# Optimization experiments

Hardware: AMD Instinct MI355X
Metric: run time of the kernel (lower is better)

The kernel has to match this reference:

```python
import jax, jax.numpy as jnp
import numpy as np

B, N, D, K = 4, 4096, 64, 16
SCALE = float(np.sqrt(D))


def setup_inputs() -> dict:
    key = jax.random.key(0)
    ks = jax.random.split(key, 16)
    f = lambda i, shape: jax.random.normal(ks[i], shape, dtype=jnp.float32) * 0.05
    return {
        'x': jax.random.normal(ks[0], (B, N, D), dtype=jnp.float32),
        'pos': jax.random.uniform(ks[1], (B, N, 3), dtype=jnp.float32),
        'Wq': f(2, (D, D)), 'Wk': f(3, (D, D)), 'Wv': f(4, (D, D)),
        'P1': f(5, (3, D)), 'p1b': f(6, (D,)), 'P2': f(7, (D, D)), 'p2b': f(8, (D,)),
        'A1': f(9, (D, D)), 'a1b': f(10, (D,)), 'A2': f(11, (D, D)), 'a2b': f(12, (D,)),
        'Wf': f(13, (D, D)), 'bf': f(14, (D,)),
    }


def _gather(feats, idx):
    # feats: [B,N,C], idx: [B,N,K] -> [B,N,K,C]  (index_points / idx_pt)
    return jax.vmap(lambda f, i: f[i])(feats, idx)


def reference(x, pos, Wq, Wk, Wv, P1, p1b, P2, p2b, A1, a1b, A2, a2b, Wf, bf):
    # kNN via squared distances (same math as square_distance + argsort[:, :, :k])
    sq = jnp.sum(pos * pos, axis=-1)                                   # [B,N]
    dists = sq[:, :, None] + sq[:, None, :] - 2.0 * jnp.einsum('bnc,bmc->bnm', pos, pos)
    _, idx = jax.lax.top_k(-dists, K)                                  # [B,N,K]

    knn_xyz = _gather(pos, idx)                                        # [B,N,K,3]
    q = x @ Wq                                                         # [B,N,D]
    kf = _gather(x @ Wk, idx)                                          # [B,N,K,D]
    v = _gather(x @ Wv, idx)                                           # [B,N,K,D]

    rel = pos[:, :, None, :] - knn_xyz                                 # [B,N,K,3]
    pos_enc = jax.nn.relu(rel @ P1 + p1b) @ P2 + p2b                   # [B,N,K,D]

    attn = jax.nn.relu((q[:, :, None, :] - kf + pos_enc) @ A1 + a1b) @ A2 + a2b
    attn = jax.nn.softmax(attn / SCALE, axis=-2)                       # softmax over K

    agg = jnp.sum(attn * (v + pos_enc), axis=2)                        # [B,N,D]
    return agg @ Wf + bf + x                                           # residual
```

## Files before the change

### kernel.cpp

```cpp
#include <hip/hip_runtime.h>
#include <hip/hip_bf16.h>
#include <stdint.h>

#define B_ 4
#define N_ 4096
#define D_ 64
#define K_ 16

static const size_t OFS_WQA1  = 0;
static const size_t OFS_WKA1  = 4096;
static const size_t OFS_WCOMB = 8192;
static const size_t OFS_C1    = 16384;
static const size_t OFS_QA1   = 16448;
static const size_t OFS_KA1   = OFS_QA1 + (size_t)B_*N_*64;
static const size_t OFS_V     = OFS_KA1 + (size_t)B_*N_*64;
static const size_t OFS_IDX   = OFS_V   + (size_t)B_*N_*64;
static const size_t OFS_POS4  = OFS_IDX + (size_t)B_*N_*16;
static const size_t OFS_BF16  = OFS_POS4 + (size_t)B_*N_*4;
static const size_t OFS_PBF   = OFS_BF16 + 6144;
static const size_t OFS_WFB   = OFS_PBF + 6144;
static const size_t OFS_APK   = OFS_WFB + 2048;
static const size_t OFS_BPK   = OFS_APK + 262144;

#define KNN_CAP 96

typedef __attribute__((ext_vector_type(8))) short short8;
typedef __attribute__((ext_vector_type(4))) float floatx4;

__device__ __forceinline__ unsigned short f2bf(float f) {
    __hip_bfloat16 h = __float2bfloat16(f);
    return *reinterpret_cast<unsigned short*>(&h);
}

__device__ __forceinline__ float bf2f(unsigned short u) {
    __hip_bfloat16 h = *reinterpret_cast<__hip_bfloat16*>(&u);
    return __bfloat162float(h);
}

__device__ __forceinline__ unsigned long long bsortu64(unsigned long long v, int l) {
#pragma unroll
    for (int k = 2; k <= 64; k <<= 1) {
#pragma unroll
        for (int j = k >> 1; j > 0; j >>= 1) {
            unsigned long long o = __shfl_xor(v, j, 64);
            unsigned long long mn = v < o ? v : o;
            unsigned long long mx = v < o ? o : v;
            v = ((((l & j) == 0) == ((l & k) == 0))) ? mn : mx;
        }
    }
    return v;
}

__device__ __forceinline__ void bsortu64x2(unsigned long long& a, unsigned long long& b, int l) {
#pragma unroll
    for (int k = 2; k <= 64; k <<= 1) {
#pragma unroll
        for (int j = k >> 1; j > 0; j >>= 1) {
            unsigned long long oa = __shfl_xor(a, j, 64);
            unsigned long long ob = __shfl_xor(b, j, 64);
            bool up = (((l & j) == 0) == ((l & k) == 0));
            unsigned long long mna = a < oa ? a : oa, mxa = a < oa ? oa : a;
            unsigned long long mnb = b < ob ? b : ob, mxb = b < ob ? ob : b;
            a = up ? mna : mxa;
            b = up ? mnb : mxb;
        }
    }
}

__global__ __launch_bounds__(256) void k_pre(
        const float* __restrict__ Wq, const float* __restrict__ Wk,
        const float* __restrict__ Wv, const float* __restrict__ Wf,
        const float* __restrict__ P2, const float* __restrict__ A1,
        const float* __restrict__ p2b, const float* __restrict__ a1b,
        const float* __restrict__ pos, float* __restrict__ ws) {
    int blk = blockIdx.x;
    unsigned short* pbf = (unsigned short*)(ws + OFS_PBF);
    if (blk < 65) {
        int i = blk * 256 + threadIdx.x;
        if (i < 4096) {
            int c = i >> 6, d = i & 63;
            float s = 0.f;
            for (int e = 0; e < 64; ++e) s = fmaf(Wq[c*64+e], A1[e*64+d], s);
            ws[OFS_WQA1 + i] = s;
            pbf[d*64 + c] = f2bf(s);
        } else if (i < 8192) {
            int j = i - 4096; int c = j >> 6, d = j & 63;
            float s = 0.f;
            for (int e = 0; e < 64; ++e) s = fmaf(Wk[c*64+e], A1[e*64+d], s);
            ws[OFS_WKA1 + j] = s;
            pbf[(64+d)*64 + c] = f2bf(s);
        } else if (i < 16384) {
            int j = i - 8192; int c = j >> 7, dd = j & 127;
            float s;
            if (dd < 64) { s = 0.f; for (int e = 0; e < 64; ++e) s = fmaf(P2[c*64+e], A1[e*64+dd], s); }
            else s = P2[c*64 + (dd - 64)];
            ws[OFS_WCOMB + j] = s;
        } else if (i < 16448) {
            int d = i - 16384;
            float s = a1b[d];
            for (int e = 0; e < 64; ++e) s = fmaf(p2b[e], A1[e*64+d], s);
            ws[OFS_C1 + d] = s;
        }
    } else if (blk < 81) {
        int i = (blk - 65) * 256 + threadIdx.x;
        int c = i >> 6, d = i & 63;
        pbf[(128+d)*64 + c] = f2bf(Wv[c*64+d]);
    } else if (blk < 97) {
        int i = (blk - 81) * 256 + threadIdx.x;
        int c = i >> 6, d = i & 63;
        ((unsigned short*)(ws + OFS_WFB))[d*64 + c] = f2bf(Wf[c*64+d]);
    } else {
        int i = (blk - 97) * 256 + threadIdx.x;
        float px = pos[(size_t)i*3+0], py = pos[(size_t)i*3+1], pz = pos[(size_t)i*3+2];
        float sq = fmaf(pz, pz, fmaf(py, py, px*px));
        ((float4*)(ws + OFS_POS4))[i] = make_float4(px, py, pz, sq);

        unsigned short xh = f2bf(px), yh = f2bf(py), zh = f2bf(pz), sh = f2bf(sq);
        float xl = px - bf2f(xh), yl = py - bf2f(yh), zl = pz - bf2f(zh), sl = sq - bf2f(sh);
        unsigned short xlb = f2bf(xl), ylb = f2bf(yl), zlb = f2bf(zl), slb = f2bf(sl);
        unsigned short m2xh = f2bf(-2.f*bf2f(xh)), m2yh = f2bf(-2.f*bf2f(yh)), m2zh = f2bf(-2.f*bf2f(zh));
        unsigned short m2xl = f2bf(-2.f*xl), m2yl = f2bf(-2.f*yl), m2zl = f2bf(-2.f*zl);
        const unsigned short ONE = 0x3F80;
        union { unsigned short u[32]; uint4 v[4]; } A, Bp;
#pragma unroll
        for (int j2 = 0; j2 < 32; ++j2) { A.u[j2] = 0; Bp.u[j2] = 0; }
        A.u[0]=m2xh; A.u[1]=m2xh; A.u[2]=m2xl;
        A.u[3]=m2yh; A.u[4]=m2yh; A.u[5]=m2yl;
        A.u[6]=m2zh; A.u[7]=m2zh; A.u[8]=m2zl;
        A.u[9]=sh;   A.u[10]=slb; A.u[11]=ONE; A.u[12]=ONE;
        Bp.u[0]=xh;  Bp.u[1]=xlb; Bp.u[2]=xh;
        Bp.u[3]=yh;  Bp.u[4]=ylb; Bp.u[5]=yh;
        Bp.u[6]=zh;  Bp.u[7]=zlb; Bp.u[8]=zh;
        Bp.u[9]=ONE; Bp.u[10]=ONE; Bp.u[11]=sh; Bp.u[12]=slb;
        uint4* ap4 = (uint4*)(ws + OFS_APK);
        uint4* bp4 = (uint4*)(ws + OFS_BPK);
#pragma unroll
        for (int j2 = 0; j2 < 4; ++j2) { ap4[(size_t)i*4+j2] = A.v[j2]; bp4[(size_t)i*4+j2] = Bp.v[j2]; }
    }
}

__global__ __launch_bounds__(256) void k_projm(const float* __restrict__ x,
                                               const float* __restrict__ A2,
                                               float* __restrict__ ws) {
    __shared__ unsigned short xT[64*72];
    __shared__ unsigned short wTs[192*72];
    const int t = threadIdx.x;
    if (blockIdx.x >= 256) {
        int i = ((int)blockIdx.x - 256) * 256 + t;
        unsigned short* wbf = (unsigned short*)(ws + OFS_BF16);
        if (i < 8192) {
            int c = i >> 7, dd = i & 127;
            wbf[dd*64 + c] = f2bf(ws[OFS_WCOMB + i]);
        } else {
            int j = i - 8192; int e = j >> 6, d = j & 63;
            wbf[8192 + d*64 + e] = f2bf(A2[j]);
        }
        return;
    }
    const unsigned short* pbf = (const unsigned short*)(ws + OFS_PBF);
    const int g0 = (int)blockIdx.x * 64;

#pragma unroll
    for (int k = 0; k < 6; ++k) {
        int id  = t + 256*k;
        int row = id >> 3, cir = id & 7;
        uint4 vv = *(const uint4*)(pbf + row*64 + cir*8);
        *(uint4*)&wTs[row*72 + cir*8] = vv;
    }
    {
        int r = t >> 2, qd = t & 3;
        const float* src = x + (size_t)(g0 + r)*64 + qd*16;
        unsigned short hb[16];
#pragma unroll
        for (int u = 0; u < 16; ++u) hb[u] = f2bf(src[u]);
        *(uint4*)&xT[r*72 + qd*16]     = *(uint4*)&hb[0];
        *(uint4*)&xT[r*72 + qd*16 + 8] = *(uint4*)&hb[8];
    }
    __syncthreads();

    const int w = t >> 6, l = t & 63, lr = l & 15, q = l >> 4;
    floatx4 acc[12];
#pragma unroll
    for (int j = 0; j < 12; ++j) acc[j] = (floatx4){0.f, 0.f, 0.f, 0.f};
#pragma unroll
    for (int kb = 0; kb < 2; ++kb) {
        short8 a = *(const short8*)&xT[(16*w + lr)*72 + 32*kb + 8*q];
#pragma unroll
        for (int j = 0; j < 12; ++j) {
            short8 bfr = *(const short8*)&wTs[(16*j + lr)*72 + 32*kb + 8*q];
            acc[j] = __builtin_amdgcn_mfma_f32_16x16x32_bf16(a, bfr, acc[j], 0, 0, 0);
        }
    }
    float* qA1 = ws + OFS_QA1;
    float* kA1 = ws + OFS_KA1;
    float* vws = ws + OFS_V;
#pragma unroll
    for (int j = 0; j < 12; ++j) {
        int col = 16*j + lr;
        float* dst = (col < 64) ? qA1 : (col < 128 ? kA1 : vws);
        int c2 = col & 63;
#pragma unroll
        for (int r = 0; r < 4; ++r) {
            int grow = g0 + 16*w + 4*q + r;
            dst[(size_t)grow*64 + c2] = acc[j][r];
        }
    }
}

__device__ __forceinline__ unsigned long long knn_pack_entry4(
        const float4 q4, const float4* __restrict__ pos4b,
        const unsigned* __restrict__ lists,
        int a1, int a2, int a3, int T, int e) {
    bool valid = e < T;
    int s = (e >= a1) + (e >= a2) + (e >= a3);
    int base = (s == 0) ? 0 : ((s == 1) ? a1 : ((s == 2) ? a2 : a3));
    int off = e - base;
    off = off < 0 ? 0 : (off > KNN_CAP-1 ? KNN_CAP-1 : off);
    unsigned idxv = lists[s*KNN_CAP + off];
    idxv = valid ? (idxv & 4095u) : 0u;
    float4 c4 = pos4b[idxv];
    float dot = fmaf(q4.z, c4.z, fmaf(q4.y, c4.y, q4.x*c4.x));
    float d = fmaxf(fmaf(-2.f, dot, q4.w + c4.w), 0.f);
    unsigned long long pk = ((unsigned long long)__float_as_uint(d) << 32) | idxv;
    return valid ? pk : ~0ull;
}

__device__ __forceinline__ unsigned long long knn_merge_rest4(
        unsigned long long best, int l, const float4 q4,
        const float4* __restrict__ pos4b, const unsigned* __restrict__ lists,
        int a1, int a2, int a3, int T) {
    for (int base = 64; base < T; base += 64) {
        unsigned long long w2 = knn_pack_entry4(q4, pos4b, lists, a1, a2, a3, T, base + l);
        w2 = bsortu64(w2, l);
        unsigned long long bb = __shfl(w2, (l - 16) & 63, 64);
        unsigned long long nv = (l < 16) ? best : ((l < 32) ? bb : ~0ull);
        best = bsortu64(nv, l);
    }
    return best;
}

__global__ __launch_bounds__(256) void k_knn(float* __restrict__ ws) {
    __shared__ unsigned surv[16*4*KNN_CAP];
    __shared__ int scnt[64];
    const unsigned short* apk = (const unsigned short*)(ws + OFS_APK);
    const unsigned short* bpk = (const unsigned short*)(ws + OFS_BPK);
    const int t = threadIdx.x;
    const int w = t >> 6, l = t & 63;
    const int lr = l & 15, hi4 = l >> 4;
    const int g0 = (int)blockIdx.x * 16;
    const int b  = g0 >> 12;

    short8 afrag = *(const short8*)(apk + (size_t)(g0 + lr)*32 + 8*hi4);
    const unsigned short* bbase = bpk + (size_t)(b*4096 + w*1024 + lr)*32 + 8*hi4;
    const floatx4 z4 = {0.f, 0.f, 0.f, 0.f};

    float run1[4], run2[4];
#pragma unroll
    for (int r = 0; r < 4; ++r) { run1[r] = 1e30f; run2[r] = 1e30f; }
    {
        short8 cur[4], nxt[4];
#pragma unroll
        for (int u = 0; u < 4; ++u) cur[u] = *(const short8*)(bbase + u*512);
#pragma unroll 4
        for (int g = 0; g < 16; ++g) {
            const int gn = ((g + 1) & 15) * 4;
#pragma unroll
            for (int u = 0; u < 4; ++u) nxt[u] = *(const short8*)(bbase + (gn+u)*512);
#pragma unroll
            for (int u = 0; u < 4; ++u) {
                floatx4 a = __builtin_amdgcn_mfma_f32_16x16x32_bf16(afrag, cur[u], z4, 0, 0, 0);
#pragma unroll
                for (int r = 0; r < 4; ++r) {
                    run2[r] = fminf(run2[r], fmaxf(run1[r], a[r]));
                    run1[r] = fminf(run1[r], a[r]);
                }
            }
#pragma unroll
            for (int u = 0; u < 4; ++u) cur[u] = nxt[u];
        }
    }

    float tau[4];
#pragma unroll
    for (int r = 0; r < 4; ++r) {
        float v = run2[r];
#pragma unroll
        for (int k = 2; k <= 16; k <<= 1) {
#pragma unroll
            for (int j = k >> 1; j > 0; j >>= 1) {
                float o = __shfl_xor(v, j, 64);
                bool up = (((lr & j) == 0) == ((lr & k) == 0));
                v = up ? fminf(v, o) : fmaxf(v, o);
            }
        }
        tau[r] = __shfl(v, (l & 48) | 7, 64) + 1e-3f;
    }

    int cnt[4] = {0, 0, 0, 0};
    const unsigned lm16 = (1u << lr) - 1u;
    unsigned su[4];
#pragma unroll
    for (int r = 0; r < 4; ++r) su[r] = (unsigned)(((4*hi4 + r)*4 + w) * KNN_CAP);
    const unsigned cand0 = (unsigned)(w*1024 + lr);
    {
        short8 cur[4], nxt[4];
#pragma unroll
        for (int u = 0; u < 4; ++u) cur[u] = *(const short8*)(bbase + u*512);
#pragma unroll 4
        for (int g = 0; g < 16; ++g) {
            const int gn = ((g + 1) & 15) * 4;
#pragma unroll
            for (int u = 0; u < 4; ++u) nxt[u] = *(const short8*)(bbase + (gn+u)*512);
#pragma unroll
            for (int u = 0; u < 4; ++u) {
                floatx4 a = __builtin_amdgcn_mfma_f32_16x16x32_bf16(afrag, cur[u], z4, 0, 0, 0);
                unsigned cid = cand0 + (unsigned)((g*4 + u)*16);
#pragma unroll
                for (int r = 0; r < 4; ++r) {
                    bool pred = a[r] <= tau[r];
                    unsigned long long m = __ballot(pred);
                    if (m) {
                        unsigned gm = (unsigned)(m >> (hi4 * 16)) & 0xFFFFu;
                        int pos = cnt[r] + __popc(gm & lm16);
                        if (pred && pos < KNN_CAP) surv[su[r] + pos] = cid;
                        cnt[r] += __popc(gm);
                    }
                }
            }
#pragma unroll
            for (int u = 0; u < 4; ++u) cur[u] = nxt[u];
        }
    }
    if (lr == 0) {
#pragma unroll
        for (int r = 0; r < 4; ++r) scnt[(4*hi4 + r)*4 + w] = cnt[r];
    }
    __syncthreads();

    const float4* pos4g = (const float4*)(ws + OFS_POS4);
    const float4* pos4b = pos4g + (size_t)b * N_;
    int* idx = (int*)(ws + OFS_IDX);
    for (int p = 0; p < 2; ++p) {
        int qa = w*4 + 2*p, qb = qa + 1;
        int ca[4], cb[4];
#pragma unroll
        for (int s = 0; s < 4; ++s) {
            int v0 = scnt[qa*4 + s]; ca[s] = v0 < KNN_CAP ? v0 : KNN_CAP;
            int v1 = scnt[qb*4 + s]; cb[s] = v1 < KNN_CAP ? v1 : KNN_CAP;
        }
        int a1 = ca[0], a2 = a1 + ca[1], a3 = a2 + ca[2], Ta = a3 + ca[3];
        int b1 = cb[0], b2 = b1 + cb[1], b3 = b2 + cb[2], Tb = b3 + cb[3];
        const unsigned* sa = surv + qa*4*KNN_CAP;
        const unsigned* sb = surv + qb*4*KNN_CAP;
        float4 q4a = pos4g[g0 + qa];
        float4 q4b = pos4g[g0 + qb];
        unsigned long long pk0 = knn_pack_entry4(q4a, pos4b, sa, a1, a2, a3, Ta, l);
        unsigned long long pk1 = knn_pack_entry4(q4b, pos4b, sb, b1, b2, b3, Tb, l);
        bsortu64x2(pk0, pk1, l);
        if (Ta > 64) pk0 = knn_merge_rest4(pk0, l, q4a, pos4b, sa, a1, a2, a3, Ta);
        if (Tb > 64) pk1 = knn_merge_rest4(pk1, l, q4b, pos4b, sb, b1, b2, b3, Tb);
        if (l < 16) {
            idx[(size_t)(g0 + qa)*16 + l] = (int)(pk0 & 0xFFFu);
            idx[(size_t)(g0 + qb)*16 + l] = (int)(pk1 & 0xFFFu);
        }
    }
}

__global__ __launch_bounds__(256) void k_attn(
    const float* __restrict__ x, const float* __restrict__ pos,
    const float* __restrict__ P1, const float* __restrict__ p1b,
    const float* __restrict__ p2b, const float* __restrict__ a2b,
    const float* __restrict__ bff, const float* __restrict__ ws,
    float* __restrict__ out) {

    __shared__ unsigned short wT[128*72];
    __shared__ unsigned short a2T[64*72];
    __shared__ unsigned short abuf[128*72];
    __shared__ float relb[128*4];
    __shared__ int   mrow[128];

    const int t  = threadIdx.x;
    const int g0 = blockIdx.x * 8;
    const int b  = g0 >> 12;
    const float* qA1 = ws + OFS_QA1;
    const float* kA1 = ws + OFS_KA1;
    const float* vws = ws + OFS_V;
    const float* c1  = ws + OFS_C1;
    const int* idx = (const int*)(ws + OFS_IDX);
    const unsigned short* wbf = (const unsigned short*)(ws + OFS_BF16);
    const unsigned short* wfb = (const unsigned short*)(ws + OFS_WFB);

#pragma unroll
    for (int k = 0; k < 6; ++k) {
        int id  = t + 256*k;
        int row = id >> 3, cir = id & 7;
        uint4 vv = *(const uint4*)(wbf + row*64 + cir*8);
        if (row < 128) *(uint4*)&wT[row*72 + cir*8] = vv;
        else           *(uint4*)&a2T[(row-128)*72 + cir*8] = vv;
    }

    if (t < 128) {
        int p = t >> 4, k = t & 15;
        int ng = g0 + p;
        int m  = idx[(size_t)ng*16 + k];
        int mg = b * N_ + m;
        mrow[t] = mg;
        relb[t*4+0] = pos[(size_t)ng*3+0] - pos[(size_t)mg*3+0];
        relb[t*4+1] = pos[(size_t)ng*3+1] - pos[(size_t)mg*3+1];
        relb[t*4+2] = pos[(size_t)ng*3+2] - pos[(size_t)mg*3+2];
    }
    __syncthreads();

    const int w = t >> 6, l = t & 63, lr = l & 15, q = l >> 4;

    float kpre[2][4][4];
    float qpre[2][4];
#pragma unroll
    for (int i = 0; i < 2; ++i) {
        int ng = g0 + 2*w + i;
#pragma unroll
        for (int j = 0; j < 4; ++j) {
            int col = 16*j + lr;
            qpre[i][j] = qA1[(size_t)ng*64 + col] + c1[col];
#pragma unroll
            for (int r = 0; r < 4; ++r) {
                int row = 32*w + 16*i + 4*q + r;
                kpre[i][j][r] = kA1[(size_t)mrow[row]*64 + col];
            }
        }
    }

    {
        int d = t & 63, r0 = t >> 6;
        float w0 = P1[d], w1 = P1[64+d], w2 = P1[128+d], bb = p1b[d];
#pragma unroll
        for (int jj = 0; jj < 32; ++jj) {
            int r = r0 + jj*4;
            float h = fmaf(relb[r*4+2], w2, fmaf(relb[r*4+1], w1, fmaf(relb[r*4+0], w0, bb)));
            abuf[r*72 + d] = f2bf(fmaxf(h, 0.f));
        }
    }
    __syncthreads();

    floatx4 acc1[2][8];
#pragma unroll
    for (int i = 0; i < 2; ++i)
#pragma unroll
        for (int j = 0; j < 8; ++j) acc1[i][j] = (floatx4){0.f, 0.f, 0.f, 0.f};
#pragma unroll
    for (int kb = 0; kb < 2; ++kb) {
        short8 a0 = *(const short8*)&abuf[(32*w      + lr)*72 + 32*kb + 8*q];
        short8 a1 = *(const short8*)&abuf[(32*w + 16 + lr)*72 + 32*kb + 8*q];
#pragma unroll
        for (int j = 0; j < 8; ++j) {
            short8 bfr = *(const short8*)&wT[(16*j + lr)*72 + 32*kb + 8*q];
            acc1[0][j] = __builtin_amdgcn_mfma_f32_16x16x32_bf16(a0, bfr, acc1[0][j], 0, 0, 0);
            acc1[1][j] = __builtin_amdgcn_mfma_f32_16x16x32_bf16(a1, bfr, acc1[1][j], 0, 0, 0);
        }
    }
    __syncthreads();

#pragma unroll
    for (int i = 0; i < 2; ++i) {
#pragma unroll
        for (int j = 0; j < 4; ++j) {
            int col = 16*j + lr;
            float qv = qpre[i][j];
#pragma unroll
            for (int r = 0; r < 4; ++r) {
                int row = 32*w + 16*i + 4*q + r;
                float t1 = acc1[i][j][r] + qv - kpre[i][j][r];
                abuf[row*72 + col] = f2bf(fmaxf(t1, 0.f));
            }
        }
    }

    float vpre[2][4][4];
#pragma unroll
    for (int i = 0; i < 2; ++i)
#pragma unroll
        for (int j = 0; j < 4; ++j) {
            int col = 16*j + lr;
#pragma unroll
            for (int r = 0; r < 4; ++r) {
                int row = 32*w + 16*i + 4*q + r;
                vpre[i][j][r] = vws[(size_t)mrow[row]*64 + col];
            }
        }
    short8 wffrag[2];
#pragma unroll
    for (int kb = 0; kb < 2; ++kb)
        wffrag[kb] = *(const short8*)&wfb[(16*w + lr)*64 + 32*kb + 8*q];
    __syncthreads();

    floatx4 acc2[2][4];
#pragma unroll
    for (int i = 0; i < 2; ++i)
#pragma unroll
        for (int j = 0; j < 4; ++j) acc2[i][j] = (floatx4){0.f, 0.f, 0.f, 0.f};
#pragma unroll
    for (int kb = 0; kb < 2; ++kb) {
        short8 a0 = *(const short8*)&abuf[(32*w      + lr)*72 + 32*kb + 8*q];
        short8 a1 = *(const short8*)&abuf[(32*w + 16 + lr)*72 + 32*kb + 8*q];
#pragma unroll
        for (int j = 0; j < 4; ++j) {
            short8 bfr = *(const short8*)&a2T[(16*j + lr)*72 + 32*kb + 8*q];
            acc2[0][j] = __builtin_amdgcn_mfma_f32_16x16x32_bf16(a0, bfr, acc2[0][j], 0, 0, 0);
            acc2[1][j] = __builtin_amdgcn_mfma_f32_16x16x32_bf16(a1, bfr, acc2[1][j], 0, 0, 0);
        }
    }
    __syncthreads();

#pragma unroll
    for (int i = 0; i < 2; ++i) {
#pragma unroll
        for (int j = 0; j < 4; ++j) {
            int col = 16*j + lr;
            float a2bv = a2b[col], p2bv = p2b[col];
            float L[4];
#pragma unroll
            for (int r = 0; r < 4; ++r) L[r] = acc2[i][j][r] + a2bv;
            float mx = fmaxf(fmaxf(L[0], L[1]), fmaxf(L[2], L[3]));
            mx = fmaxf(mx, __shfl_xor(mx, 16, 64));
            mx = fmaxf(mx, __shfl_xor(mx, 32, 64));
            float ssum = 0.f, part = 0.f;
#pragma unroll
            for (int r = 0; r < 4; ++r) {
                float e = __expf((L[r] - mx) * 0.125f);
                ssum += e;
                float wv = vpre[i][j][r] + (acc1[i][4+j][r] + p2bv);
                part = fmaf(e, wv, part);
            }
            ssum += __shfl_xor(ssum, 16, 64);
            ssum += __shfl_xor(ssum, 32, 64);
            part += __shfl_xor(part, 16, 64);
            part += __shfl_xor(part, 32, 64);
            float agg = part / ssum;
            if (q == 0) abuf[(2*w + i)*72 + col] = f2bf(agg);
        }
    }
    __syncthreads();

    {
        floatx4 accF = (floatx4){0.f, 0.f, 0.f, 0.f};
#pragma unroll
        for (int kb = 0; kb < 2; ++kb) {
            short8 afr = *(const short8*)&abuf[lr*72 + 32*kb + 8*q];
            accF = __builtin_amdgcn_mfma_f32_16x16x32_bf16(afr, wffrag[kb], accF, 0, 0, 0);
        }
        if (q < 2) {
            int col = 16*w + lr;
            float bv = bff[col];
#pragma unroll
            for (int r = 0; r < 4; ++r) {
                int g = g0 + 4*q + r;
                out[(size_t)g*64 + col] = accF[r] + bv + x[(size_t)g*64 + col];
            }
        }
    }
}

extern "C" void kernel_launch(void* const* d_in, const int* in_sizes, int n_in,
                              void* d_out, int out_size, void* d_ws, size_t ws_size,
                              hipStream_t stream) {
    const float* x   = (const float*)d_in[0];
    const float* pos = (const float*)d_in[1];
    const float* Wq  = (const float*)d_in[2];
    const float* Wk  = (const float*)d_in[3];
    const float* Wv  = (const float*)d_in[4];
    const float* P1  = (const float*)d_in[5];
    const float* p1b = (const float*)d_in[6];
    const float* P2  = (const float*)d_in[7];
    const float* p2b = (const float*)d_in[8];
    const float* A1  = (const float*)d_in[9];
    const float* a1b = (const float*)d_in[10];
    const float* A2  = (const float*)d_in[11];
    const float* a2b = (const float*)d_in[12];
    const float* Wf  = (const float*)d_in[13];
    const float* bf  = (const float*)d_in[14];
    float* out = (float*)d_out;
    float* ws  = (float*)d_ws;

    hipLaunchKernelGGL(k_pre,   dim3(161),  dim3(256), 0, stream,
                       Wq, Wk, Wv, Wf, P2, A1, p2b, a1b, pos, ws);
    hipLaunchKernelGGL(k_projm, dim3(304),  dim3(256), 0, stream, x, A2, ws);
    hipLaunchKernelGGL(k_knn,   dim3(1024), dim3(256), 0, stream, ws);
    hipLaunchKernelGGL(k_attn,  dim3(2048), dim3(256), 0, stream,
                       x, pos, P1, p1b, p2b, a2b, bf, ws, out);
}
```

Before: 195.2 us.

## Split kNN candidate scan across 8 waves with shared-memory min merge and atomic survivors

The kNN kernel now runs 512 threads, so each of 8 waves scans 512 candidates instead of 4 waves scanning 1024. Per-wave top-2 minima are merged through shared memory to form the threshold. Survivors go into one list per query via LDS atomics instead of per-wave ballot-compacted lists, which removes the 4-list indexing in the final sort. The aim is shorter per-wave serial scans and more parallelism, at the cost of an extra barrier, LDS atomic contention, and the survivor cap now applying to the whole list rather than to each wave's list.

```diff
diff --git a/kernel.cpp b/kernel.cpp
--- a/kernel.cpp
+++ b/kernel.cpp
@@ -207,16 +207,12 @@
     }
 }
 
-__device__ __forceinline__ unsigned long long knn_pack_entry4(
+__device__ __forceinline__ unsigned long long knn_entry(
         const float4 q4, const float4* __restrict__ pos4b,
-        const unsigned* __restrict__ lists,
-        int a1, int a2, int a3, int T, int e) {
+        const unsigned* __restrict__ s, int T, int e) {
     bool valid = e < T;
-    int s = (e >= a1) + (e >= a2) + (e >= a3);
-    int base = (s == 0) ? 0 : ((s == 1) ? a1 : ((s == 2) ? a2 : a3));
-    int off = e - base;
-    off = off < 0 ? 0 : (off > KNN_CAP-1 ? KNN_CAP-1 : off);
-    unsigned idxv = lists[s*KNN_CAP + off];
+    int re = e < KNN_CAP ? e : KNN_CAP - 1;
+    unsigned idxv = s[re];
     idxv = valid ? (idxv & 4095u) : 0u;
     float4 c4 = pos4b[idxv];
     float dot = fmaf(q4.z, c4.z, fmaf(q4.y, c4.y, q4.x*c4.x));
@@ -225,12 +221,11 @@
     return valid ? pk : ~0ull;
 }
 
-__device__ __forceinline__ unsigned long long knn_merge_rest4(
+__device__ __forceinline__ unsigned long long knn_merge_rest1(
         unsigned long long best, int l, const float4 q4,
-        const float4* __restrict__ pos4b, const unsigned* __restrict__ lists,
-        int a1, int a2, int a3, int T) {
+        const float4* __restrict__ pos4b, const unsigned* __restrict__ s, int T) {
     for (int base = 64; base < T; base += 64) {
-        unsigned long long w2 = knn_pack_entry4(q4, pos4b, lists, a1, a2, a3, T, base + l);
+        unsigned long long w2 = knn_entry(q4, pos4b, s, T, base + l);
         w2 = bsortu64(w2, l);
         unsigned long long bb = __shfl(w2, (l - 16) & 63, 64);
         unsigned long long nv = (l < 16) ? best : ((l < 32) ? bb : ~0ull);
@@ -239,9 +234,11 @@
     return best;
 }
 
-__global__ __launch_bounds__(256) void k_knn(float* __restrict__ ws) {
-    __shared__ unsigned surv[16*4*KNN_CAP];
-    __shared__ int scnt[64];
+__global__ __launch_bounds__(512, 8) void k_knn(float* __restrict__ ws) {
+    __shared__ float2 minbuf[16*16*9];
+    __shared__ unsigned surv[16*KNN_CAP];
+    __shared__ int   scnt[16];
+    __shared__ float taubuf[16];
     const unsigned short* apk = (const unsigned short*)(ws + OFS_APK);
     const unsigned short* bpk = (const unsigned short*)(ws + OFS_BPK);
     const int t = threadIdx.x;
@@ -250,24 +247,26 @@
     const int g0 = (int)blockIdx.x * 16;
     const int b  = g0 >> 12;
 
+    if (t < 16) scnt[t] = 0;
+
     short8 afrag = *(const short8*)(apk + (size_t)(g0 + lr)*32 + 8*hi4);
-    const unsigned short* bbase = bpk + (size_t)(b*4096 + w*1024 + lr)*32 + 8*hi4;
+    const unsigned short* bbase = bpk + (size_t)(b*4096 + w*512 + lr)*32 + 8*hi4;
     const floatx4 z4 = {0.f, 0.f, 0.f, 0.f};
 
     float run1[4], run2[4];
 #pragma unroll
     for (int r = 0; r < 4; ++r) { run1[r] = 1e30f; run2[r] = 1e30f; }
     {
-        short8 cur[4], nxt[4];
-#pragma unroll
-        for (int u = 0; u < 4; ++u) cur[u] = *(const short8*)(bbase + u*512);
+        short8 cur[2], nxt[2];
+#pragma unroll
+        for (int u = 0; u < 2; ++u) cur[u] = *(const short8*)(bbase + u*512);
 #pragma unroll 4
         for (int g = 0; g < 16; ++g) {
-            const int gn = ((g + 1) & 15) * 4;
-#pragma unroll
-            for (int u = 0; u < 4; ++u) nxt[u] = *(const short8*)(bbase + (gn+u)*512);
-#pragma unroll
-            for (int u = 0; u < 4; ++u) {
+            const int gn = ((g + 1) & 15) * 2;
+#pragma unroll
+            for (int u = 0; u < 2; ++u) nxt[u] = *(const short8*)(bbase + (gn+u)*512);
+#pragma unroll
+            for (int u = 0; u < 2; ++u) {
                 floatx4 a = __builtin_amdgcn_mfma_f32_16x16x32_bf16(afrag, cur[u], z4, 0, 0, 0);
 #pragma unroll
                 for (int r = 0; r < 4; ++r) {
@@ -276,93 +275,88 @@
                 }
             }
 #pragma unroll
-            for (int u = 0; u < 4; ++u) cur[u] = nxt[u];
-        }
-    }
-
-    float tau[4];
-#pragma unroll
-    for (int r = 0; r < 4; ++r) {
-        float v = run2[r];
+            for (int u = 0; u < 2; ++u) cur[u] = nxt[u];
+        }
+    }
+#pragma unroll
+    for (int r = 0; r < 4; ++r)
+        minbuf[((4*hi4 + r)*16 + lr)*9 + w] = make_float2(run1[r], run2[r]);
+    __syncthreads();
+
+    if (t < 256) {
+        int q = t >> 4, cl = t & 15;
+        float m1 = 1e30f, m2 = 1e30f;
+#pragma unroll
+        for (int wv = 0; wv < 8; ++wv) {
+            float2 p = minbuf[(q*16 + cl)*9 + wv];
+            float hi = fmaxf(m1, p.x);
+            m1 = fminf(m1, p.x);
+            m2 = fminf(fminf(m2, p.y), hi);
+        }
+        float v = m2;
 #pragma unroll
         for (int k = 2; k <= 16; k <<= 1) {
 #pragma unroll
             for (int j = k >> 1; j > 0; j >>= 1) {
                 float o = __shfl_xor(v, j, 64);
-                bool up = (((lr & j) == 0) == ((lr & k) == 0));
+                bool up = (((cl & j) == 0) == ((cl & k) == 0));
                 v = up ? fminf(v, o) : fmaxf(v, o);
             }
         }
-        tau[r] = __shfl(v, (l & 48) | 7, 64) + 1e-3f;
-    }
-
-    int cnt[4] = {0, 0, 0, 0};
-    const unsigned lm16 = (1u << lr) - 1u;
-    unsigned su[4];
-#pragma unroll
-    for (int r = 0; r < 4; ++r) su[r] = (unsigned)(((4*hi4 + r)*4 + w) * KNN_CAP);
-    const unsigned cand0 = (unsigned)(w*1024 + lr);
+        if (cl == 7) taubuf[q] = v + 1e-3f;
+    }
+    __syncthreads();
+
+    float tau[4];
+#pragma unroll
+    for (int r = 0; r < 4; ++r) tau[r] = taubuf[4*hi4 + r];
+
+    const unsigned cand0 = (unsigned)(w*512 + lr);
     {
-        short8 cur[4], nxt[4];
-#pragma unroll
-        for (int u = 0; u < 4; ++u) cur[u] = *(const short8*)(bbase + u*512);
+        short8 cur[2], nxt[2];
+#pragma unroll
+        for (int u = 0; u < 2; ++u) cur[u] = *(const short8*)(bbase + u*512);
 #pragma unroll 4
         for (int g = 0; g < 16; ++g) {
-            const int gn = ((g + 1) & 15) * 4;
-#pragma unroll
-            for (int u = 0; u < 4; ++u) nxt[u] = *(const short8*)(bbase + (gn+u)*512);
-#pragma unroll
-            for (int u = 0; u < 4; ++u) {
+            const int gn = ((g + 1) & 15) * 2;
+#pragma unroll
+            for (int u = 0; u < 2; ++u) nxt[u] = *(const short8*)(bbase + (gn+u)*512);
+#pragma unroll
+            for (int u = 0; u < 2; ++u) {
                 floatx4 a = __builtin_amdgcn_mfma_f32_16x16x32_bf16(afrag, cur[u], z4, 0, 0, 0);
-                unsigned cid = cand0 + (unsigned)((g*4 + u)*16);
+                unsigned cid = cand0 + (unsigned)((g*2 + u)*16);
 #pragma unroll
                 for (int r = 0; r < 4; ++r) {
-                    bool pred = a[r] <= tau[r];
-                    unsigned long long m = __ballot(pred);
-                    if (m) {
-                        unsigned gm = (unsigned)(m >> (hi4 * 16)) & 0xFFFFu;
-                        int pos = cnt[r] + __popc(gm & lm16);
-                        if (pred && pos < KNN_CAP) surv[su[r] + pos] = cid;
-                        cnt[r] += __popc(gm);
+                    if (a[r] <= tau[r]) {
+                        int p = atomicAdd(&scnt[4*hi4 + r], 1);
+                        if (p < KNN_CAP) surv[(4*hi4 + r)*KNN_CAP + p] = cid;
                     }
                 }
             }
 #pragma unroll
-            for (int u = 0; u < 4; ++u) cur[u] = nxt[u];
-        }
-    }
-    if (lr == 0) {
-#pragma unroll
-        for (int r = 0; r < 4; ++r) scnt[(4*hi4 + r)*4 + w] = cnt[r];
+            for (int u = 0; u < 2; ++u) cur[u] = nxt[u];
+        }
     }
     __syncthreads();
 
     const float4* pos4g = (const float4*)(ws + OFS_POS4);
     const float4* pos4b = pos4g + (size_t)b * N_;
     int* idx = (int*)(ws + OFS_IDX);
-    for (int p = 0; p < 2; ++p) {
-        int qa = w*4 + 2*p, qb = qa + 1;
-        int ca[4], cb[4];
-#pragma unroll
-        for (int s = 0; s < 4; ++s) {
-            int v0 = scnt[qa*4 + s]; ca[s] = v0 < KNN_CAP ? v0 : KNN_CAP;
-            int v1 = scnt[qb*4 + s]; cb[s] = v1 < KNN_CAP ? v1 : KNN_CAP;
-        }
-        int a1 = ca[0], a2 = a1 + ca[1], a3 = a2 + ca[2], Ta = a3 + ca[3];
-        int b1 = cb[0], b2 = b1 + cb[1], b3 = b2 + cb[2], Tb = b3 + cb[3];
-        const unsigned* sa = surv + qa*4*KNN_CAP;
-        const unsigned* sb = surv + qb*4*KNN_CAP;
-        float4 q4a = pos4g[g0 + qa];
-        float4 q4b = pos4g[g0 + qb];
-        unsigned long long pk0 = knn_pack_entry4(q4a, pos4b, sa, a1, a2, a3, Ta, l);
-        unsigned long long pk1 = knn_pack_entry4(q4b, pos4b, sb, b1, b2, b3, Tb, l);
-        bsortu64x2(pk0, pk1, l);
-        if (Ta > 64) pk0 = knn_merge_rest4(pk0, l, q4a, pos4b, sa, a1, a2, a3, Ta);
-        if (Tb > 64) pk1 = knn_merge_rest4(pk1, l, q4b, pos4b, sb, b1, b2, b3, Tb);
-        if (l < 16) {
-            idx[(size_t)(g0 + qa)*16 + l] = (int)(pk0 & 0xFFFu);
-            idx[(size_t)(g0 + qb)*16 + l] = (int)(pk1 & 0xFFFu);
-        }
+    int qa = 2*w, qb = 2*w + 1;
+    int Ta = scnt[qa]; Ta = Ta < KNN_CAP ? Ta : KNN_CAP;
+    int Tb = scnt[qb]; Tb = Tb < KNN_CAP ? Tb : KNN_CAP;
+    const unsigned* sa = surv + qa*KNN_CAP;
+    const unsigned* sb = surv + qb*KNN_CAP;
+    float4 q4a = pos4g[g0 + qa];
+    float4 q4b = pos4g[g0 + qb];
+    unsigned long long pk0 = knn_entry(q4a, pos4b, sa, Ta, l);
+    unsigned long long pk1 = knn_entry(q4b, pos4b, sb, Tb, l);
+    bsortu64x2(pk0, pk1, l);
+    if (Ta > 64) pk0 = knn_merge_rest1(pk0, l, q4a, pos4b, sa, Ta);
+    if (Tb > 64) pk1 = knn_merge_rest1(pk1, l, q4b, pos4b, sb, Tb);
+    if (l < 16) {
+        idx[(size_t)(g0 + qa)*16 + l] = (int)(pk0 & 0xFFFu);
+        idx[(size_t)(g0 + qb)*16 + l] = (int)(pk1 & 0xFFFu);
     }
 }
 
@@ -584,7 +578,7 @@
     hipLaunchKernelGGL(k_pre,   dim3(161),  dim3(256), 0, stream,
                        Wq, Wk, Wv, Wf, P2, A1, p2b, a1b, pos, ws);
     hipLaunchKernelGGL(k_projm, dim3(304),  dim3(256), 0, stream, x, A2, ws);
-    hipLaunchKernelGGL(k_knn,   dim3(1024), dim3(256), 0, stream, ws);
+    hipLaunchKernelGGL(k_knn,   dim3(1024), dim3(512), 0, stream, ws);
     hipLaunchKernelGGL(k_attn,  dim3(2048), dim3(256), 0, stream,
                        x, pos, P1, p1b, p2b, a2b, bf, ws, out);
 }
```

Result: faster. 170.7 us (-12.6%).
